# Performance work log

Measured on AMD Instinct MI355X. Metric: run time of the kernel, lower is better.

The kernel has to match this reference:

```python
import jax, jax.numpy as jnp
import numpy as np

N = 50000      # nodes
E = 800000     # edges (before self-loops)
IN = 128       # in_dim
HID = 64       # hidden_dim
HEADS = 4
OUT = 64       # out_dim
NEG_SLOPE = 0.2
EPS = 1e-16


def gat_conv(x, src, dst, W, att_src, att_dst, b, heads, out_ch, concat):
    """PyG GATConv (eval mode): gather -> attention -> segment softmax -> scatter."""
    n = x.shape[0]
    h = (x @ W).reshape(n, heads, out_ch)                 # [N,H,C]
    a_s = (h * att_src).sum(-1)                           # [N,H]
    a_d = (h * att_dst).sum(-1)                           # [N,H]
    alpha = jax.nn.leaky_relu(a_s[src] + a_d[dst], NEG_SLOPE)   # [E,H]
    amax = jax.ops.segment_max(alpha, dst, num_segments=n)      # stable softmax per dst
    alpha = jnp.exp(alpha - amax[dst])
    denom = jax.ops.segment_sum(alpha, dst, num_segments=n)
    alpha = alpha / (denom[dst] + EPS)
    msg = h[src] * alpha[:, :, None]                      # [E,H,C]
    out = jax.ops.segment_sum(msg, dst, num_segments=n)   # [N,H,C]
    out = out.reshape(n, heads * out_ch) if concat else out.mean(axis=1)
    return out + b


def setup_inputs() -> dict:
    key = jax.random.key(0)
    ks = jax.random.split(key, 16)
    lin = lambda k, fi, fo: jax.random.normal(k, (fi, fo), jnp.float32) / jnp.sqrt(fi)
    x = jax.random.normal(ks[0], (N, IN), jnp.float32)
    edge_index = jax.random.randint(ks[1], (2, E), 0, N, dtype=jnp.int32)
    return {
        "x": x,
        "edge_index": edge_index,
        "W1": lin(ks[2], IN, HEADS * HID),
        "att_src1": jax.random.normal(ks[3], (HEADS, HID)) * 0.1,
        "att_dst1": jax.random.normal(ks[4], (HEADS, HID)) * 0.1,
        "b1": jnp.zeros((HEADS * HID,), jnp.float32),
        "W2": lin(ks[5], HEADS * HID, OUT),
        "att_src2": jax.random.normal(ks[6], (1, OUT)) * 0.1,
        "att_dst2": jax.random.normal(ks[7], (1, OUT)) * 0.1,
        "b2": jnp.zeros((OUT,), jnp.float32),
        "dW1": lin(ks[8], OUT, HID),
        "db1": jnp.zeros((HID,), jnp.float32),
        "dW2": lin(ks[9], HID, IN),
        "db2": jnp.zeros((IN,), jnp.float32),
    }


def reference(x, edge_index, W1, att_src1, att_dst1, b1, W2, att_src2, att_dst2, b2,
              dW1, db1, dW2, db2):
    n = x.shape[0]
    loops = jnp.arange(n, dtype=edge_index.dtype)         # add_self_loops (PyG default)
    src = jnp.concatenate([edge_index[0], loops])
    dst = jnp.concatenate([edge_index[1], loops])
    # encode (dropout is identity in eval mode)
    h = jax.nn.elu(gat_conv(x, src, dst, W1, att_src1, att_dst1, b1, HEADS, HID, True))
    z = gat_conv(h, src, dst, W2, att_src2, att_dst2, b2, 1, OUT, False)
    # F.normalize(z, p=2, dim=-1)
    z = z / jnp.clip(jnp.linalg.norm(z, axis=-1, keepdims=True), 1e-12)
    # feat_decoder: Linear -> ELU -> Linear
    x_hat = jax.nn.elu(z @ dW1 + db1) @ dW2 + db2
    return (z, x_hat)
```

## Files before the change

### kernel.cpp

```cpp
#include <hip/hip_runtime.h>
#include <hip/hip_bf16.h>


#define IN_DIM   128
#define C1       256
#define HEADS    4
#define HID      64
#define OUT_DIM  64

typedef __attribute__((ext_vector_type(8))) short short8;
typedef __attribute__((ext_vector_type(4))) float f32x4;
typedef __attribute__((ext_vector_type(2))) float f32x2;

__device__ __forceinline__ float lrelu(float x) { return x > 0.f ? x : 0.2f * x; }
__device__ __forceinline__ float elu1(float x)  { return x > 0.f ? x : (__expf(x) - 1.f); }
__device__ __forceinline__ float expc(float x)  { return __expf(fminf(x, 60.f)); }
__device__ __forceinline__ float bfu(unsigned int u) {
    union { unsigned int i; float f; } c; c.i = u << 16; return c.f;
}
__device__ __forceinline__ unsigned short pk(float f) {
    union { float f; unsigned int i; } c; c.f = f;
    return (unsigned short)((c.i + 0x7fffu + ((c.i >> 16) & 1u)) >> 16);
}
__device__ __forceinline__ void pkfma_lo(f32x2& acc, const f32x2 x, const f32x2 wp) {
    asm("v_pk_fma_f32 %0, %1, %2, %0 op_sel_hi:[1,0,1]"
        : "+v"(acc) : "v"(x), "v"(wp));
}
__device__ __forceinline__ void pkfma_hi(f32x2& acc, const f32x2 x, const f32x2 wp) {
    asm("v_pk_fma_f32 %0, %1, %2, %0 op_sel:[0,1,0] op_sel_hi:[1,1,1]"
        : "+v"(acc) : "v"(x), "v"(wp));
}
__device__ __forceinline__ f32x2 bf2up(unsigned int u) {
    union { unsigned int i[2]; f32x2 f; } c;
    c.i[0] = u << 16;
    c.i[1] = u & 0xffff0000u;
    return c.f;
}

__global__ __launch_bounds__(256) void w1f_k(const float* __restrict__ W1,
                                             const float* __restrict__ W2,
                                             const float* __restrict__ as1,
                                             const float* __restrict__ ad1,
                                             unsigned short* __restrict__ W1f,
                                             unsigned short* __restrict__ W2f,
                                             float* __restrict__ u_s,
                                             float* __restrict__ u_d)
{
    const int b = blockIdx.x;
    if (b == 16) {
        for (int idx = threadIdx.x; idx < 512; idx += 256) {
            const int h = idx >> 7, k = idx & 127;
            float ss = 0.f, dd = 0.f;
            #pragma unroll 4
            for (int c = 0; c < 64; ++c) {
                const float wv = W1[k * 256 + h * 64 + c];
                ss += wv * as1[h * 64 + c];
                dd += wv * ad1[h * 64 + c];
            }
            u_s[idx] = ss;
            u_d[idx] = dd;
        }
        return;
    }
    if (b >= 17) {
        const int idx = (b - 17) * 256 + threadIdx.x;
        if (idx >= 32 * 64) return;
        const int lane = idx & 63, e = idx >> 6;
        const int nt = e >> 3, kc = e & 7, q = lane >> 4, c = lane & 15;
        unsigned short tmp[8];
        #pragma unroll
        for (int j = 0; j < 8; ++j)
            tmp[j] = pk(W2[(kc * 32 + q * 8 + j) * 64 + nt * 16 + c]);
        ushort4* dst = (ushort4*)(W2f + (size_t)idx * 8);
        dst[0] = make_ushort4(tmp[0], tmp[1], tmp[2], tmp[3]);
        dst[1] = make_ushort4(tmp[4], tmp[5], tmp[6], tmp[7]);
        return;
    }
    const int idx = b * 256 + threadIdx.x;
    if (idx >= 64 * 64) return;
    const int lane = idx & 63, e = idx >> 6;
    const int nt = e >> 2, kc = e & 3, q = lane >> 4, c = lane & 15;
    unsigned short tmp[8];
    #pragma unroll
    for (int j = 0; j < 8; ++j)
        tmp[j] = pk(W1[(kc * 32 + q * 8 + j) * 256 + nt * 16 + c]);
    ushort4* dst = (ushort4*)(W1f + (size_t)idx * 8);
    dst[0] = make_ushort4(tmp[0], tmp[1], tmp[2], tmp[3]);
    dst[1] = make_ushort4(tmp[4], tmp[5], tmp[6], tmp[7]);
}

__global__ __launch_bounds__(256) void xprep_k(
    const float* __restrict__ x, const float* __restrict__ u_s,
    const float* __restrict__ u_d, unsigned short* __restrict__ xb,
    float* __restrict__ a_s1, float* __restrict__ a_d1, int N)
{
    __shared__ float us[512], ud[512];
    const int t = threadIdx.x;
    for (int i = t; i < 512; i += 256) { us[i] = u_s[i]; ud[i] = u_d[i]; }
    __syncthreads();
    const int w = t >> 6, l = t & 63;
    const int n = blockIdx.x * 4 + w;
    if (n >= N) return;
    const float2 xv = *(const float2*)&x[(size_t)n * IN_DIM + 2 * l];
    const unsigned int p2 =
        (unsigned int)pk(xv.x) | ((unsigned int)pk(xv.y) << 16);
    *(unsigned int*)&xb[(size_t)n * IN_DIM + 2 * l] = p2;
    #pragma unroll
    for (int h = 0; h < 4; ++h) {
        float ps = xv.x * us[h * 128 + 2 * l] + xv.y * us[h * 128 + 2 * l + 1];
        float pd = xv.x * ud[h * 128 + 2 * l] + xv.y * ud[h * 128 + 2 * l + 1];
        #pragma unroll
        for (int off = 1; off < 64; off <<= 1) {
            ps += __shfl_xor(ps, off, 64);
            pd += __shfl_xor(pd, off, 64);
        }
        if (l == 0) {
            a_s1[n * 4 + h] = ps;
            a_d1[n * 4 + h] = pd;
        }
    }
}

__global__ __launch_bounds__(256) void deg_k(const int* __restrict__ ei, int E,
                                             int Etot, int* __restrict__ rowptr,
                                             int N)
{
    const int bin = blockIdx.x & 7;
    const int chunk = blockIdx.x >> 3, nchunk = gridDim.x >> 3;
    const int per = (Etot + nchunk - 1) / nchunk;
    const int e0 = chunk * per, e1 = min(e0 + per, Etot);
    const int lo = (int)(((long long)N * bin) >> 3);
    const int hi = (int)(((long long)N * (bin + 1)) >> 3);
    for (int e = e0 + threadIdx.x; e < e1; e += 256) {
        const int d = (e < E) ? ei[E + e] : e - E;
        if (d >= lo && d < hi) atomicAdd(&rowptr[1 + d], 1);
    }
}

__device__ __forceinline__ int blk_incl_scan(int v, int t) {
    __shared__ int wsum[4];
    const int lane = t & 63, wid = t >> 6;
    int s = v;
    #pragma unroll
    for (int off = 1; off < 64; off <<= 1) {
        const int u = __shfl_up(s, off, 64);
        if (lane >= off) s += u;
    }
    if (lane == 63) wsum[wid] = s;
    __syncthreads();
    int add = 0;
    #pragma unroll
    for (int k = 0; k < 4; ++k) if (k < wid) add += wsum[k];
    __syncthreads();
    return s + add;
}

__global__ __launch_bounds__(256) void scanA_k(const int* __restrict__ rowptr,
                                               int* __restrict__ psum, int N)
{
    const int t = threadIdx.x;
    const int i = blockIdx.x * 256 + t;
    int v = (i < N) ? rowptr[1 + i] : 0;
    #pragma unroll
    for (int off = 1; off < 64; off <<= 1) v += __shfl_xor(v, off, 64);
    __shared__ int ws[4];
    if ((t & 63) == 0) ws[t >> 6] = v;
    __syncthreads();
    if (t == 0) psum[blockIdx.x] = ws[0] + ws[1] + ws[2] + ws[3];
}

__global__ __launch_bounds__(256) void scanB_k(int* __restrict__ psum, int SC)
{
    const int t = threadIdx.x;
    const int v = (t < SC) ? psum[t] : 0;
    const int inc = blk_incl_scan(v, t);
    if (t < SC) psum[t] = inc - v;
}

__global__ __launch_bounds__(256) void scanC_k(int* __restrict__ rowptr,
                                               int* __restrict__ cursor,
                                               const int* __restrict__ psum, int N)
{
    const int t = threadIdx.x;
    const int i = blockIdx.x * 256 + t;
    const int v = (i < N) ? rowptr[1 + i] : 0;
    const int inc = blk_incl_scan(v, t);
    const int base = psum[blockIdx.x];
    if (i < N) {
        rowptr[1 + i] = base + inc;
        cursor[i]     = base + inc - v;
    }
}

__global__ __launch_bounds__(256) void fill_k(const int* __restrict__ ei, int E,
                                              int Etot, int* __restrict__ cursor,
                                              int* __restrict__ col, int N)
{
    const int bin = blockIdx.x & 7;
    const int chunk = blockIdx.x >> 3, nchunk = gridDim.x >> 3;
    const int per = (Etot + nchunk - 1) / nchunk;
    const int e0 = chunk * per, e1 = min(e0 + per, Etot);
    const int lo = (int)(((long long)N * bin) >> 3);
    const int hi = (int)(((long long)N * (bin + 1)) >> 3);
    for (int e = e0 + threadIdx.x; e < e1; e += 256) {
        const int d = (e < E) ? ei[E + e] : e - E;
        if (d >= lo && d < hi) {
            const int s = (e < E) ? ei[e] : d;
            const int pos = atomicAdd(&cursor[d], 1);
            col[pos] = s;
        }
    }
}

__global__ __launch_bounds__(256) void agg1x_k(
    const int* __restrict__ rowptr, const int* __restrict__ col,
    const float* __restrict__ a_s1, const float* __restrict__ a_d1,
    const unsigned short* __restrict__ xb, unsigned short* __restrict__ xagg,
    int N)
{
    __shared__ int    scolS[4][64];
    __shared__ float4 w4S[4][64];
    const int t = threadIdx.x, w = t >> 6, l = t & 63;
    const int n = blockIdx.x * 4 + w;
    if (n >= N) return;
    const int beg = rowptr[n], end = rowptr[n + 1];
    const float4 dv = *(const float4*)&a_d1[n * 4];
    float4 ws = {0.f, 0.f, 0.f, 0.f};
    f32x2 acc[4] = {{0.f,0.f},{0.f,0.f},{0.f,0.f},{0.f,0.f}};
    const unsigned short* xbl = xb + 2 * l;
    for (int t0 = beg; t0 < end; t0 += 64) {
        const int m = min(64, end - t0);
        const int p = t0 + l;
        int sc = 0;
        float4 wv = {0.f, 0.f, 0.f, 0.f};
        if (p < end) {
            sc = col[p];
            const float4 av = *(const float4*)&a_s1[sc * 4];
            wv.x = expc(lrelu(av.x + dv.x));
            wv.y = expc(lrelu(av.y + dv.y));
            wv.z = expc(lrelu(av.z + dv.z));
            wv.w = expc(lrelu(av.w + dv.w));
            ws.x += wv.x; ws.y += wv.y; ws.z += wv.z; ws.w += wv.w;
        }
        scolS[w][l] = sc;
        w4S[w][l]   = wv;
        __threadfence_block();
        for (int j0 = 0; j0 < m; j0 += 16) {
            const int4 s0 = *(const int4*)&scolS[w][j0];
            const int4 s1 = *(const int4*)&scolS[w][j0 + 4];
            const int4 s2 = *(const int4*)&scolS[w][j0 + 8];
            const int4 s3 = *(const int4*)&scolS[w][j0 + 12];
            const int su[16] = {s0.x, s0.y, s0.z, s0.w, s1.x, s1.y, s1.z, s1.w,
                                s2.x, s2.y, s2.z, s2.w, s3.x, s3.y, s3.z, s3.w};
            unsigned int hv[16];
            #pragma unroll
            for (int u = 0; u < 16; ++u)
                hv[u] = *(const unsigned int*)(xbl + (size_t)su[u] * IN_DIM);
            #pragma unroll
            for (int u = 0; u < 16; ++u) {
                const float* wb = (const float*)&w4S[w][j0 + u];
                const f32x2 wp01 = *(const f32x2*)(wb);
                const f32x2 wp23 = *(const f32x2*)(wb + 2);
                const f32x2 xv = bf2up(hv[u]);
                pkfma_lo(acc[0], xv, wp01);
                pkfma_hi(acc[1], xv, wp01);
                pkfma_lo(acc[2], xv, wp23);
                pkfma_hi(acc[3], xv, wp23);
            }
        }
    }
    #pragma unroll
    for (int off = 1; off < 64; off <<= 1) {
        ws.x += __shfl_xor(ws.x, off, 64);
        ws.y += __shfl_xor(ws.y, off, 64);
        ws.z += __shfl_xor(ws.z, off, 64);
        ws.w += __shfl_xor(ws.w, off, 64);
    }
    const float i0 = 1.f / (ws.x + 1e-16f), i1 = 1.f / (ws.y + 1e-16f);
    const float i2 = 1.f / (ws.z + 1e-16f), i3 = 1.f / (ws.w + 1e-16f);
    unsigned short* out = xagg + (size_t)n * 512 + 2 * l;
    *(unsigned int*)(out)       = (unsigned int)pk(acc[0][0] * i0) |
                                  ((unsigned int)pk(acc[0][1] * i0) << 16);
    *(unsigned int*)(out + 128) = (unsigned int)pk(acc[1][0] * i1) |
                                  ((unsigned int)pk(acc[1][1] * i1) << 16);
    *(unsigned int*)(out + 256) = (unsigned int)pk(acc[2][0] * i2) |
                                  ((unsigned int)pk(acc[2][1] * i2) << 16);
    *(unsigned int*)(out + 384) = (unsigned int)pk(acc[3][0] * i3) |
                                  ((unsigned int)pk(acc[3][1] * i3) << 16);
}

__global__ __launch_bounds__(256) void gemm1b_k(
    const unsigned short* __restrict__ xagg, const unsigned short* __restrict__ W1f,
    const float* __restrict__ b1, unsigned short* __restrict__ hxb, int N)
{
    __shared__ short lds[64 * 264];
    const int t = threadIdx.x, w = t >> 6, l = t & 63;
    const int q = l >> 4, c = l & 15;
    const int n0 = blockIdx.x * 64;
    const int arow = 16 * w + c;
    f32x4 acc[16];
    #pragma unroll
    for (int nt = 0; nt < 16; ++nt) acc[nt] = (f32x4){0.f, 0.f, 0.f, 0.f};
    #pragma unroll
    for (int half = 0; half < 2; ++half) {
        if (half) __syncthreads();
        for (int i = t; i < 64 * 32; i += 256) {
            const int r = i >> 5, ch = (i & 31) * 8;
            const int rn = min(n0 + r, N - 1);
            *(short8*)&lds[r * 264 + ch] =
                *(const short8*)&xagg[(size_t)rn * 512 + half * 256 + ch];
        }
        __syncthreads();
        #pragma unroll
        for (int hh = 0; hh < 2; ++hh) {
            const int h = half * 2 + hh;
            short8 afr[4];
            #pragma unroll
            for (int kc = 0; kc < 4; ++kc)
                afr[kc] = *(const short8*)&lds[arow * 264 + hh * 128 + kc * 32 + q * 8];
            #pragma unroll
            for (int nt = 0; nt < 4; ++nt) {
                #pragma unroll
                for (int kc = 0; kc < 4; ++kc) {
                    const short8 bfr = *(const short8*)(W1f +
                        ((size_t)((h * 4 + nt) * 4 + kc) * 64 + l) * 8);
                    acc[h * 4 + nt] = __builtin_amdgcn_mfma_f32_16x16x32_bf16(
                        afr[kc], bfr, acc[h * 4 + nt], 0, 0, 0);
                }
            }
        }
    }
    __syncthreads();
    #pragma unroll
    for (int nt = 0; nt < 16; ++nt)
        #pragma unroll
        for (int r = 0; r < 4; ++r) {
            const float v = elu1(acc[nt][r] + b1[nt * 16 + c]);
            lds[(16 * w + q * 4 + r) * 264 + nt * 16 + c] = (short)pk(v);
        }
    __syncthreads();
    for (int i = t; i < 64 * 32; i += 256) {
        const int r = i >> 5, ch = (i & 31) * 8;
        const int node = n0 + r;
        if (node < N)
            *(short8*)&hxb[(size_t)node * C1 + ch] =
                *(const short8*)&lds[r * 264 + ch];
    }
}

__global__ __launch_bounds__(256) void gemm2_k(
    const unsigned short* __restrict__ hxb, const unsigned short* __restrict__ W2f,
    const float* __restrict__ as2, const float* __restrict__ ad2,
    unsigned short* __restrict__ h2b, float* __restrict__ a_s2,
    float* __restrict__ a_d2, int N)
{
    __shared__ short lds[64 * 264];
    const int t = threadIdx.x, w = t >> 6, l = t & 63;
    const int q = l >> 4, c = l & 15;
    const int n0 = blockIdx.x * 64;
    for (int i = t; i < 64 * 32; i += 256) {
        const int r = i >> 5, ch = (i & 31) * 8;
        const int rn = min(n0 + r, N - 1);
        *(short8*)&lds[r * 264 + ch] =
            *(const short8*)&hxb[(size_t)rn * C1 + ch];
    }
    __syncthreads();
    short8 afr[8];
    const int arow = 16 * w + c;
    #pragma unroll
    for (int kc = 0; kc < 8; ++kc)
        afr[kc] = *(const short8*)&lds[arow * 264 + kc * 32 + q * 8];
    f32x4 acc[4];
    #pragma unroll
    for (int nt = 0; nt < 4; ++nt) acc[nt] = (f32x4){0.f, 0.f, 0.f, 0.f};
    #pragma unroll
    for (int nt = 0; nt < 4; ++nt) {
        #pragma unroll
        for (int kc = 0; kc < 8; ++kc) {
            const short8 bfr =
                *(const short8*)(W2f + ((size_t)(nt * 8 + kc) * 64 + l) * 8);
            acc[nt] = __builtin_amdgcn_mfma_f32_16x16x32_bf16(afr[kc], bfr,
                                                              acc[nt], 0, 0, 0);
        }
    }
    {
        float vsr[4] = {0.f, 0.f, 0.f, 0.f}, vdr[4] = {0.f, 0.f, 0.f, 0.f};
        #pragma unroll
        for (int nt = 0; nt < 4; ++nt) {
            const float sa = as2[nt * 16 + c], da = ad2[nt * 16 + c];
            #pragma unroll
            for (int r = 0; r < 4; ++r) {
                vsr[r] += acc[nt][r] * sa;
                vdr[r] += acc[nt][r] * da;
            }
        }
        #pragma unroll
        for (int r = 0; r < 4; ++r) {
            #pragma unroll
            for (int off = 1; off < 16; off <<= 1) {
                vsr[r] += __shfl_xor(vsr[r], off, 64);
                vdr[r] += __shfl_xor(vdr[r], off, 64);
            }
            const int node = n0 + 16 * w + q * 4 + r;
            if (c == 0 && node < N) {
                a_s2[node] = vsr[r];
                a_d2[node] = vdr[r];
            }
        }
    }
    __syncthreads();
    #pragma unroll
    for (int nt = 0; nt < 4; ++nt)
        #pragma unroll
        for (int r = 0; r < 4; ++r)
            lds[(16 * w + q * 4 + r) * 72 + nt * 16 + c] = (short)pk(acc[nt][r]);
    __syncthreads();
    for (int i = t; i < 64 * 8; i += 256) {
        const int r = i >> 3, ch = (i & 7) * 8;
        const int node = n0 + r;
        if (node < N)
            *(short8*)&h2b[(size_t)node * OUT_DIM + ch] =
                *(const short8*)&lds[r * 72 + ch];
    }
}

__global__ __launch_bounds__(256) void agg2_k(
    const int* __restrict__ rowptr, const int* __restrict__ col,
    const float* __restrict__ a_s2, const float* __restrict__ a_d2,
    const unsigned short* __restrict__ h2b, const float* __restrict__ b2,
    float* __restrict__ zout, int N)
{
    __shared__ int2 swS[4][64];
    const int t = threadIdx.x, w = t >> 6, l = t & 63;
    const int n = blockIdx.x * 4 + w;
    if (n >= N) return;
    const int beg = rowptr[n], end = rowptr[n + 1];
    const float dn = a_d2[n];
    const int half = l >> 5, c2 = l & 31;
    f32x2 acc = {0.f, 0.f};
    float wsum = 0.f;
    const unsigned short* h2l = h2b + 2 * c2;
    for (int t0 = beg; t0 < end; t0 += 64) {
        const int m = min(64, end - t0);
        const int p = t0 + l;
        int sc = 0; float wv = 0.f;
        if (p < end) {
            sc = col[p];
            wv = expc(lrelu(a_s2[sc] + dn));
            wsum += wv;
        }
        swS[w][l] = make_int2(sc, __float_as_int(wv));
        __threadfence_block();
        const int pairs = (m + 1) >> 1;
        for (int j0 = 0; j0 < pairs; j0 += 8) {
            int2 sv[8];
            #pragma unroll
            for (int u = 0; u < 8; ++u)
                sv[u] = swS[w][2 * (j0 + u) + half];
            unsigned int hv[8];
            #pragma unroll
            for (int u = 0; u < 8; ++u)
                hv[u] = *(const unsigned int*)(h2l + (size_t)sv[u].x * OUT_DIM);
            #pragma unroll
            for (int u = 0; u < 8; ++u) {
                union { int2 i; f32x2 f; } cv; cv.i = sv[u];
                pkfma_hi(acc, bf2up(hv[u]), cv.f);
            }
        }
    }
    float a0 = acc[0], a1 = acc[1];
    a0 += __shfl_xor(a0, 32, 64);
    a1 += __shfl_xor(a1, 32, 64);
    #pragma unroll
    for (int off = 1; off < 64; off <<= 1) wsum += __shfl_xor(wsum, off, 64);
    const float inv = 1.f / (wsum + 1e-16f);
    float z0 = a0 * inv + b2[2 * c2];
    float z1 = a1 * inv + b2[2 * c2 + 1];
    float sq = z0 * z0 + z1 * z1;
    #pragma unroll
    for (int off = 1; off < 32; off <<= 1) sq += __shfl_xor(sq, off, 64);
    const float rn = 1.f / fmaxf(sqrtf(sq), 1e-12f);
    if (l < 32) {
        float2 o; o.x = z0 * rn; o.y = z1 * rn;
        *(float2*)&zout[(size_t)n * OUT_DIM + 2 * c2] = o;
    }
}

__global__ __launch_bounds__(256) void dec_k(
    const float* __restrict__ z,
    const float* __restrict__ dW1, const float* __restrict__ db1,
    const float* __restrict__ dW2, const float* __restrict__ db2,
    float* __restrict__ xhat, int N)
{
    __shared__ float zs[32 * 64];
    __shared__ float ts[32 * 64];
    const int t = threadIdx.x;
    const int n0 = blockIdx.x * 32;
    for (int i = t; i < 32 * 64; i += 256) {
        const int nb_l = i >> 6, k = i & 63;
        const int n = min(n0 + nb_l, N - 1);
        zs[(nb_l >> 3) * 512 + k * 8 + (nb_l & 7)] = z[(size_t)n * OUT_DIM + k];
    }
    __syncthreads();
    const int w = t >> 6, l = t & 63;
    const float* zw = zs + w * 512;
    float* tw = ts + w * 512;
    float acc[8] = {0.f, 0.f, 0.f, 0.f, 0.f, 0.f, 0.f, 0.f};
    #pragma unroll 4
    for (int k = 0; k < 64; ++k) {
        const float wv = dW1[k * HID + l];
        const float4 xa = *(const float4*)&zw[k * 8];
        const float4 xb = *(const float4*)&zw[k * 8 + 4];
        acc[0] += xa.x * wv; acc[1] += xa.y * wv;
        acc[2] += xa.z * wv; acc[3] += xa.w * wv;
        acc[4] += xb.x * wv; acc[5] += xb.y * wv;
        acc[6] += xb.z * wv; acc[7] += xb.w * wv;
    }
    const float bb = db1[l];
    #pragma unroll
    for (int nb = 0; nb < 8; ++nb) tw[l * 8 + nb] = elu1(acc[nb] + bb);
    __syncthreads();
    float a0[8] = {0.f, 0.f, 0.f, 0.f, 0.f, 0.f, 0.f, 0.f};
    float a1[8] = {0.f, 0.f, 0.f, 0.f, 0.f, 0.f, 0.f, 0.f};
    #pragma unroll 2
    for (int k = 0; k < 64; ++k) {
        const float w0 = dW2[k * IN_DIM + l];
        const float w1 = dW2[k * IN_DIM + 64 + l];
        const float4 xa = *(const float4*)&tw[k * 8];
        const float4 xb = *(const float4*)&tw[k * 8 + 4];
        const float xv[8] = {xa.x, xa.y, xa.z, xa.w, xb.x, xb.y, xb.z, xb.w};
        #pragma unroll
        for (int nb = 0; nb < 8; ++nb) {
            a0[nb] += xv[nb] * w0;
            a1[nb] += xv[nb] * w1;
        }
    }
    const float bb0 = db2[l], bb1 = db2[64 + l];
    #pragma unroll
    for (int nb = 0; nb < 8; ++nb) {
        const int n = n0 + w * 8 + nb;
        if (n >= N) break;
        xhat[(size_t)n * IN_DIM + l]      = a0[nb] + bb0;
        xhat[(size_t)n * IN_DIM + 64 + l] = a1[nb] + bb1;
    }
}

extern "C" void kernel_launch(void* const* d_in, const int* in_sizes, int n_in,
                              void* d_out, int out_size, void* d_ws, size_t ws_size,
                              hipStream_t stream)
{
    const float* x   = (const float*)d_in[0];
    const int*   ei  = (const int*)d_in[1];
    const float* W1  = (const float*)d_in[2];
    const float* as1 = (const float*)d_in[3];
    const float* ad1 = (const float*)d_in[4];
    const float* b1  = (const float*)d_in[5];
    const float* W2  = (const float*)d_in[6];
    const float* as2 = (const float*)d_in[7];
    const float* ad2 = (const float*)d_in[8];
    const float* b2  = (const float*)d_in[9];
    const float* dW1 = (const float*)d_in[10];
    const float* db1 = (const float*)d_in[11];
    const float* dW2 = (const float*)d_in[12];
    const float* db2 = (const float*)d_in[13];

    const int N    = in_sizes[0] / IN_DIM;
    const int E    = in_sizes[1] / 2;
    const int Etot = E + N;

    unsigned short* W1f = (unsigned short*)d_ws;
    unsigned short* W2f = W1f + 32768;
    float* u_s = (float*)(W2f + 16384);
    float* u_d = u_s + 512;
    unsigned short* hxb  = (unsigned short*)(u_d + 512);
    unsigned short* xagg = hxb  + (size_t)N * C1;
    unsigned short* xb   = xagg + (size_t)N * 512;
    unsigned short* h2b  = xb   + (size_t)N * IN_DIM;
    float* a_s1 = (float*)(h2b + (size_t)N * OUT_DIM);
    float* a_d1 = a_s1 + (size_t)N * HEADS;
    float* a_s2 = a_d1 + (size_t)N * HEADS;
    float* a_d2 = a_s2 + (size_t)N;
    int* rowptr = (int*)(a_d2 + (size_t)N);
    int* cursor = rowptr + (N + 1);
    int* col    = cursor + N;
    int* psum   = col + Etot;

    const size_t needed = (size_t)N * 1968 + (size_t)Etot * 4 + 103428;
    if (ws_size < needed) return;

    hipMemsetAsync(rowptr, 0, (size_t)(N + 1) * sizeof(int), stream);

    const int SC    = (N + 255) / 256;
    const int mblk  = (N + 63) / 64;
    const int nblk4 = (N + 3) / 4;
    const int nchunk = (Etot + 2047) / 2048;
    const int bgrid  = nchunk * 8;
    w1f_k   <<<25, 256, 0, stream>>>(W1, W2, as1, ad1, W1f, W2f, u_s, u_d);
    xprep_k <<<nblk4, 256, 0, stream>>>(x, u_s, u_d, xb, a_s1, a_d1, N);
    deg_k   <<<bgrid, 256, 0, stream>>>(ei, E, Etot, rowptr, N);
    scanA_k <<<SC, 256, 0, stream>>>(rowptr, psum, N);
    scanB_k <<<1, 256, 0, stream>>>(psum, SC);
    scanC_k <<<SC, 256, 0, stream>>>(rowptr, cursor, psum, N);
    fill_k  <<<bgrid, 256, 0, stream>>>(ei, E, Etot, cursor, col, N);
    agg1x_k <<<nblk4, 256, 0, stream>>>(rowptr, col, a_s1, a_d1, xb, xagg, N);
    gemm1b_k<<<mblk, 256, 0, stream>>>(xagg, W1f, b1, hxb, N);
    gemm2_k <<<mblk, 256, 0, stream>>>(hxb, W2f, as2, ad2, h2b, a_s2, a_d2, N);
    agg2_k  <<<nblk4, 256, 0, stream>>>(rowptr, col, a_s2, a_d2, h2b, b2,
                                        (float*)d_out, N);
    dec_k   <<<(N + 31) / 32, 256, 0, stream>>>((const float*)d_out, dW1, db1,
                                                dW2, db2,
                                                (float*)d_out + (size_t)N * OUT_DIM, N);
}
```

Baseline: 361.6 us.

## Fuse gemm1/gemm2, merge degree count into xprep, fold scanB, halve agg1 unroll

Merges the two dense GEMM kernels so the layer-1 hidden activations stay in LDS and never round-trip through global memory. The degree-count pass is folded into the x-prep launch as extra blocks. The single-block scanB is removed by having each scanC block sum the preceding partial sums itself. The agg1 gather unroll is cut from 16 to 8 edges per step, which trades memory-level parallelism for lower register pressure. Together these cut launch count and global traffic but add redundant prefix work in every scan block.

```diff
diff --git a/kernel.cpp b/kernel.cpp
--- a/kernel.cpp
+++ b/kernel.cpp
@@ -89,11 +89,27 @@
     dst[1] = make_ushort4(tmp[4], tmp[5], tmp[6], tmp[7]);
 }
 
-__global__ __launch_bounds__(256) void xprep_k(
+__global__ __launch_bounds__(256) void xprep_deg_k(
     const float* __restrict__ x, const float* __restrict__ u_s,
     const float* __restrict__ u_d, unsigned short* __restrict__ xb,
-    float* __restrict__ a_s1, float* __restrict__ a_d1, int N)
-{
+    float* __restrict__ a_s1, float* __restrict__ a_d1, int N,
+    const int* __restrict__ ei, int E, int Etot, int* __restrict__ rowptr,
+    int nblk4, int nchunk)
+{
+    if (blockIdx.x >= nblk4) {
+        const int bb = blockIdx.x - nblk4;
+        const int bin = bb & 7;
+        const int chunk = bb >> 3;
+        const int per = (Etot + nchunk - 1) / nchunk;
+        const int e0 = chunk * per, e1 = min(e0 + per, Etot);
+        const int lo = (int)(((long long)N * bin) >> 3);
+        const int hi = (int)(((long long)N * (bin + 1)) >> 3);
+        for (int e = e0 + threadIdx.x; e < e1; e += 256) {
+            const int d = (e < E) ? ei[E + e] : e - E;
+            if (d >= lo && d < hi) atomicAdd(&rowptr[1 + d], 1);
+        }
+        return;
+    }
     __shared__ float us[512], ud[512];
     const int t = threadIdx.x;
     for (int i = t; i < 512; i += 256) { us[i] = u_s[i]; ud[i] = u_d[i]; }
@@ -121,22 +137,6 @@
     }
 }
 
-__global__ __launch_bounds__(256) void deg_k(const int* __restrict__ ei, int E,
-                                             int Etot, int* __restrict__ rowptr,
-                                             int N)
-{
-    const int bin = blockIdx.x & 7;
-    const int chunk = blockIdx.x >> 3, nchunk = gridDim.x >> 3;
-    const int per = (Etot + nchunk - 1) / nchunk;
-    const int e0 = chunk * per, e1 = min(e0 + per, Etot);
-    const int lo = (int)(((long long)N * bin) >> 3);
-    const int hi = (int)(((long long)N * (bin + 1)) >> 3);
-    for (int e = e0 + threadIdx.x; e < e1; e += 256) {
-        const int d = (e < E) ? ei[E + e] : e - E;
-        if (d >= lo && d < hi) atomicAdd(&rowptr[1 + d], 1);
-    }
-}
-
 __device__ __forceinline__ int blk_incl_scan(int v, int t) {
     __shared__ int wsum[4];
     const int lane = t & 63, wid = t >> 6;
@@ -169,23 +169,23 @@
     if (t == 0) psum[blockIdx.x] = ws[0] + ws[1] + ws[2] + ws[3];
 }
 
-__global__ __launch_bounds__(256) void scanB_k(int* __restrict__ psum, int SC)
-{
-    const int t = threadIdx.x;
-    const int v = (t < SC) ? psum[t] : 0;
-    const int inc = blk_incl_scan(v, t);
-    if (t < SC) psum[t] = inc - v;
-}
-
 __global__ __launch_bounds__(256) void scanC_k(int* __restrict__ rowptr,
                                                int* __restrict__ cursor,
-                                               const int* __restrict__ psum, int N)
+                                               const int* __restrict__ psum,
+                                               int N, int SC)
 {
     const int t = threadIdx.x;
+    int s = (t < SC && t < (int)blockIdx.x) ? psum[t] : 0;
+    #pragma unroll
+    for (int off = 1; off < 64; off <<= 1) s += __shfl_xor(s, off, 64);
+    __shared__ int bsum[4];
+    if ((t & 63) == 0) bsum[t >> 6] = s;
+    __syncthreads();
+    const int base = bsum[0] + bsum[1] + bsum[2] + bsum[3];
+    __syncthreads();
     const int i = blockIdx.x * 256 + t;
     const int v = (i < N) ? rowptr[1 + i] : 0;
     const int inc = blk_incl_scan(v, t);
-    const int base = psum[blockIdx.x];
     if (i < N) {
         rowptr[1 + i] = base + inc;
         cursor[i]     = base + inc - v;
@@ -245,19 +245,16 @@
         scolS[w][l] = sc;
         w4S[w][l]   = wv;
         __threadfence_block();
-        for (int j0 = 0; j0 < m; j0 += 16) {
+        for (int j0 = 0; j0 < m; j0 += 8) {
             const int4 s0 = *(const int4*)&scolS[w][j0];
             const int4 s1 = *(const int4*)&scolS[w][j0 + 4];
-            const int4 s2 = *(const int4*)&scolS[w][j0 + 8];
-            const int4 s3 = *(const int4*)&scolS[w][j0 + 12];
-            const int su[16] = {s0.x, s0.y, s0.z, s0.w, s1.x, s1.y, s1.z, s1.w,
-                                s2.x, s2.y, s2.z, s2.w, s3.x, s3.y, s3.z, s3.w};
-            unsigned int hv[16];
-            #pragma unroll
-            for (int u = 0; u < 16; ++u)
+            const int su[8] = {s0.x, s0.y, s0.z, s0.w, s1.x, s1.y, s1.z, s1.w};
+            unsigned int hv[8];
+            #pragma unroll
+            for (int u = 0; u < 8; ++u)
                 hv[u] = *(const unsigned int*)(xbl + (size_t)su[u] * IN_DIM);
             #pragma unroll
-            for (int u = 0; u < 16; ++u) {
+            for (int u = 0; u < 8; ++u) {
                 const float* wb = (const float*)&w4S[w][j0 + u];
                 const f32x2 wp01 = *(const f32x2*)(wb);
                 const f32x2 wp23 = *(const f32x2*)(wb + 2);
@@ -289,9 +286,12 @@
                                   ((unsigned int)pk(acc[3][1] * i3) << 16);
 }
 
-__global__ __launch_bounds__(256) void gemm1b_k(
+__global__ __launch_bounds__(256) void gemm12_k(
     const unsigned short* __restrict__ xagg, const unsigned short* __restrict__ W1f,
-    const float* __restrict__ b1, unsigned short* __restrict__ hxb, int N)
+    const float* __restrict__ b1, const unsigned short* __restrict__ W2f,
+    const float* __restrict__ as2, const float* __restrict__ ad2,
+    unsigned short* __restrict__ h2b, float* __restrict__ a_s2,
+    float* __restrict__ a_d2, int N)
 {
     __shared__ short lds[64 * 264];
     const int t = threadIdx.x, w = t >> 6, l = t & 63;
@@ -339,48 +339,21 @@
             lds[(16 * w + q * 4 + r) * 264 + nt * 16 + c] = (short)pk(v);
         }
     __syncthreads();
-    for (int i = t; i < 64 * 32; i += 256) {
-        const int r = i >> 5, ch = (i & 31) * 8;
-        const int node = n0 + r;
-        if (node < N)
-            *(short8*)&hxb[(size_t)node * C1 + ch] =
-                *(const short8*)&lds[r * 264 + ch];
-    }
-}
-
-__global__ __launch_bounds__(256) void gemm2_k(
-    const unsigned short* __restrict__ hxb, const unsigned short* __restrict__ W2f,
-    const float* __restrict__ as2, const float* __restrict__ ad2,
-    unsigned short* __restrict__ h2b, float* __restrict__ a_s2,
-    float* __restrict__ a_d2, int N)
-{
-    __shared__ short lds[64 * 264];
-    const int t = threadIdx.x, w = t >> 6, l = t & 63;
-    const int q = l >> 4, c = l & 15;
-    const int n0 = blockIdx.x * 64;
-    for (int i = t; i < 64 * 32; i += 256) {
-        const int r = i >> 5, ch = (i & 31) * 8;
-        const int rn = min(n0 + r, N - 1);
-        *(short8*)&lds[r * 264 + ch] =
-            *(const short8*)&hxb[(size_t)rn * C1 + ch];
-    }
-    __syncthreads();
-    short8 afr[8];
-    const int arow = 16 * w + c;
+    short8 afr2[8];
     #pragma unroll
     for (int kc = 0; kc < 8; ++kc)
-        afr[kc] = *(const short8*)&lds[arow * 264 + kc * 32 + q * 8];
-    f32x4 acc[4];
-    #pragma unroll
-    for (int nt = 0; nt < 4; ++nt) acc[nt] = (f32x4){0.f, 0.f, 0.f, 0.f};
+        afr2[kc] = *(const short8*)&lds[arow * 264 + kc * 32 + q * 8];
+    f32x4 acc2[4];
+    #pragma unroll
+    for (int nt = 0; nt < 4; ++nt) acc2[nt] = (f32x4){0.f, 0.f, 0.f, 0.f};
     #pragma unroll
     for (int nt = 0; nt < 4; ++nt) {
         #pragma unroll
         for (int kc = 0; kc < 8; ++kc) {
             const short8 bfr =
                 *(const short8*)(W2f + ((size_t)(nt * 8 + kc) * 64 + l) * 8);
-            acc[nt] = __builtin_amdgcn_mfma_f32_16x16x32_bf16(afr[kc], bfr,
-                                                              acc[nt], 0, 0, 0);
+            acc2[nt] = __builtin_amdgcn_mfma_f32_16x16x32_bf16(afr2[kc], bfr,
+                                                               acc2[nt], 0, 0, 0);
         }
     }
     {
@@ -390,8 +363,8 @@
             const float sa = as2[nt * 16 + c], da = ad2[nt * 16 + c];
             #pragma unroll
             for (int r = 0; r < 4; ++r) {
-                vsr[r] += acc[nt][r] * sa;
-                vdr[r] += acc[nt][r] * da;
+                vsr[r] += acc2[nt][r] * sa;
+                vdr[r] += acc2[nt][r] * da;
             }
         }
         #pragma unroll
@@ -413,7 +386,7 @@
     for (int nt = 0; nt < 4; ++nt)
         #pragma unroll
         for (int r = 0; r < 4; ++r)
-            lds[(16 * w + q * 4 + r) * 72 + nt * 16 + c] = (short)pk(acc[nt][r]);
+            lds[(16 * w + q * 4 + r) * 72 + nt * 16 + c] = (short)pk(acc2[nt][r]);
     __syncthreads();
     for (int i = t; i < 64 * 8; i += 256) {
         const int r = i >> 3, ch = (i & 7) * 8;
@@ -572,8 +545,7 @@
     unsigned short* W2f = W1f + 32768;
     float* u_s = (float*)(W2f + 16384);
     float* u_d = u_s + 512;
-    unsigned short* hxb  = (unsigned short*)(u_d + 512);
-    unsigned short* xagg = hxb  + (size_t)N * C1;
+    unsigned short* xagg = (unsigned short*)(u_d + 512);
     unsigned short* xb   = xagg + (size_t)N * 512;
     unsigned short* h2b  = xb   + (size_t)N * IN_DIM;
     float* a_s1 = (float*)(h2b + (size_t)N * OUT_DIM);
@@ -585,7 +557,7 @@
     int* col    = cursor + N;
     int* psum   = col + Etot;
 
-    const size_t needed = (size_t)N * 1968 + (size_t)Etot * 4 + 103428;
+    const size_t needed = (size_t)N * 1456 + (size_t)Etot * 4 + 103432;
     if (ws_size < needed) return;
 
     hipMemsetAsync(rowptr, 0, (size_t)(N + 1) * sizeof(int), stream);
@@ -595,19 +567,19 @@
     const int nblk4 = (N + 3) / 4;
     const int nchunk = (Etot + 2047) / 2048;
     const int bgrid  = nchunk * 8;
-    w1f_k   <<<25, 256, 0, stream>>>(W1, W2, as1, ad1, W1f, W2f, u_s, u_d);
-    xprep_k <<<nblk4, 256, 0, stream>>>(x, u_s, u_d, xb, a_s1, a_d1, N);
-    deg_k   <<<bgrid, 256, 0, stream>>>(ei, E, Etot, rowptr, N);
-    scanA_k <<<SC, 256, 0, stream>>>(rowptr, psum, N);
-    scanB_k <<<1, 256, 0, stream>>>(psum, SC);
-    scanC_k <<<SC, 256, 0, stream>>>(rowptr, cursor, psum, N);
-    fill_k  <<<bgrid, 256, 0, stream>>>(ei, E, Etot, cursor, col, N);
-    agg1x_k <<<nblk4, 256, 0, stream>>>(rowptr, col, a_s1, a_d1, xb, xagg, N);
-    gemm1b_k<<<mblk, 256, 0, stream>>>(xagg, W1f, b1, hxb, N);
-    gemm2_k <<<mblk, 256, 0, stream>>>(hxb, W2f, as2, ad2, h2b, a_s2, a_d2, N);
-    agg2_k  <<<nblk4, 256, 0, stream>>>(rowptr, col, a_s2, a_d2, h2b, b2,
-                                        (float*)d_out, N);
-    dec_k   <<<(N + 31) / 32, 256, 0, stream>>>((const float*)d_out, dW1, db1,
-                                                dW2, db2,
-                                                (float*)d_out + (size_t)N * OUT_DIM, N);
-}
+    w1f_k     <<<25, 256, 0, stream>>>(W1, W2, as1, ad1, W1f, W2f, u_s, u_d);
+    xprep_deg_k<<<nblk4 + bgrid, 256, 0, stream>>>(x, u_s, u_d, xb, a_s1, a_d1,
+                                                   N, ei, E, Etot, rowptr,
+                                                   nblk4, nchunk);
+    scanA_k   <<<SC, 256, 0, stream>>>(rowptr, psum, N);
+    scanC_k   <<<SC, 256, 0, stream>>>(rowptr, cursor, psum, N, SC);
+    fill_k    <<<bgrid, 256, 0, stream>>>(ei, E, Etot, cursor, col, N);
+    agg1x_k   <<<nblk4, 256, 0, stream>>>(rowptr, col, a_s1, a_d1, xb, xagg, N);
+    gemm12_k  <<<mblk, 256, 0, stream>>>(xagg, W1f, b1, W2f, as2, ad2, h2b,
+                                         a_s2, a_d2, N);
+    agg2_k    <<<nblk4, 256, 0, stream>>>(rowptr, col, a_s2, a_d2, h2b, b2,
+                                          (float*)d_out, N);
+    dec_k     <<<(N + 31) / 32, 256, 0, stream>>>((const float*)d_out, dW1, db1,
+                                                  dW2, db2,
+                                                  (float*)d_out + (size_t)N * OUT_DIM, N);
+}
```

After: 338.7 us. -6.3%, faster.
